# Kernel tuning notes

Measured on AMD Instinct MI355X. Metric: run time of the kernel, lower is better.

Reference implementation:

```python
import jax, jax.numpy as jnp
import numpy as np

B, S_EN, S_FR, EMB, UNITS, V_EN, V_FR = 64, 64, 64, 512, 1024, 32000, 16000


def setup_inputs() -> dict:
    key = jax.random.key(0)
    ks = jax.random.split(key, 16)
    sc = 0.05
    inp = {
        "en": jax.random.randint(ks[0], (B, S_EN), 0, V_EN, dtype=jnp.int32),
        "fr": jax.random.randint(ks[1], (B, S_FR), 0, V_FR, dtype=jnp.int32),
        "valid_len": jax.random.randint(ks[2], (B,), 1, S_EN, dtype=jnp.int32),
        "en_emb": jax.random.normal(ks[3], (V_EN, EMB), jnp.float32) * sc,
        "de_emb": jax.random.normal(ks[4], (V_FR, EMB), jnp.float32) * sc,
        "en_W": jax.random.normal(ks[5], (EMB, 4 * UNITS), jnp.float32) * sc,
        "en_U": jax.random.normal(ks[6], (UNITS, 4 * UNITS), jnp.float32) * sc,
        "en_b": jnp.zeros((4 * UNITS,), jnp.float32),
        "de_W": jax.random.normal(ks[7], (UNITS + EMB, 4 * UNITS), jnp.float32) * sc,
        "de_U": jax.random.normal(ks[8], (UNITS, 4 * UNITS), jnp.float32) * sc,
        "de_b": jnp.zeros((4 * UNITS,), jnp.float32),
        "Wq": jax.random.normal(ks[9], (UNITS, UNITS), jnp.float32) * sc,
        "Wk": jax.random.normal(ks[10], (UNITS, UNITS), jnp.float32) * sc,
        "wv": jax.random.normal(ks[11], (UNITS, 1), jnp.float32) * sc,
        "Wd": jax.random.normal(ks[12], (UNITS, V_FR), jnp.float32) * sc,
        "bd": jnp.zeros((V_FR,), jnp.float32),
    }
    return inp


def _lstm_step(h, c, x, W, Uw, b):
    # keras gate order: i, f, g(candidate), o
    z = x @ W + h @ Uw + b
    i, f, g, o = jnp.split(z, 4, axis=-1)
    c = jax.nn.sigmoid(f) * c + jax.nn.sigmoid(i) * jnp.tanh(g)
    h = jax.nn.sigmoid(o) * jnp.tanh(c)
    return h, c


def reference(en, fr, valid_len, en_emb, de_emb, en_W, en_U, en_b,
              de_W, de_U, de_b, Wq, Wk, wv, Wd, bd):
    b = en.shape[0]
    u = en_U.shape[0]
    # ----- Encode -----
    x_en = en_emb[en]                       # (B, S_en, E)
    h0 = jnp.zeros((b, u), x_en.dtype)

    def enc_step(carry, xt):
        h, c = carry
        h, c = _lstm_step(h, c, xt, en_W, en_U, en_b)
        return (h, c), h

    (h, c), en_o = jax.lax.scan(enc_step, (h0, h0), jnp.swapaxes(x_en, 0, 1))
    en_o = jnp.swapaxes(en_o, 0, 1)         # (B, S_en, U)

    # ----- Decode with additive attention per step -----
    kproj = en_o @ Wk                       # (B, S_en, U), key proj is step-invariant
    pos = jnp.arange(en.shape[1])
    attn_mask = pos[None, :] < valid_len[:, None]   # (B, S_en)
    x_fr = de_emb[fr]                       # (B, S_fr, E)

    def dec_step(carry, xt):
        h, c = carry
        q = h @ Wq                          # (B, U)
        feat = jnp.tanh(q[:, None, :] + kproj)      # (B, S_en, U)
        score = jnp.squeeze(feat @ wv, -1)          # (B, S_en)
        score = jnp.where(attn_mask, score, -1000000.0)
        attn = jax.nn.softmax(score, axis=-1)
        context = jnp.einsum('bs,bsu->bu', attn, en_o)
        x = jnp.concatenate([context, xt], axis=-1)  # (B, U+E)
        h, c = _lstm_step(h, c, x, de_W, de_U, de_b)
        return (h, c), h

    (_, _), hs = jax.lax.scan(dec_step, (h, c), jnp.swapaxes(x_fr, 0, 1))
    logits = jnp.swapaxes(hs, 0, 1) @ Wd + bd       # (B, S_fr, V_fr)
    return logits
```

## Files before the change

### kernel.cpp

```cpp
#include <hip/hip_runtime.h>
#include <math.h>

#define BD    64
#define SEQ   64
#define EMBD  512
#define UNITS 1024
#define NG    4096
#define VFR   16000

typedef __attribute__((ext_vector_type(8))) short bf16x8;
typedef __attribute__((ext_vector_type(4))) float f32x4;

__device__ __forceinline__ float sigm(float x) { return 1.0f / (1.0f + __expf(-x)); }
__device__ __forceinline__ float tanh_f(float x) {
    float e = __expf(2.0f * x);
    return 1.0f - 2.0f / (e + 1.0f);
}
__device__ __forceinline__ unsigned bf16bits(float v) {
    unsigned u = __float_as_uint(v);
    return (u + 0x7FFFu + ((u >> 16) & 1u)) >> 16;
}
__device__ __forceinline__ float bf2f(short s) {
    return __uint_as_float(((unsigned)(unsigned short)s) << 16);
}
__device__ __forceinline__ void split2(float v, short& h, short& l) {
    unsigned hb = bf16bits(v);
    float hv = __uint_as_float(hb << 16);
    h = (short)hb;
    l = (short)bf16bits(v - hv);
}

__device__ __forceinline__ void gbar(int* cnt, int* gen, int nb) {
    __threadfence();
    __syncthreads();
    if (threadIdx.x == 0) {
        int g = __hip_atomic_load(gen, __ATOMIC_RELAXED, __HIP_MEMORY_SCOPE_AGENT);
        if (atomicAdd(cnt, 1) == nb - 1) {
            __hip_atomic_store(cnt, 0, __ATOMIC_RELAXED, __HIP_MEMORY_SCOPE_AGENT);
            __hip_atomic_store(gen, g + 1, __ATOMIC_RELEASE, __HIP_MEMORY_SCOPE_AGENT);
        } else {
            while (__hip_atomic_load(gen, __ATOMIC_RELAXED, __HIP_MEMORY_SCOPE_AGENT) == g)
                __builtin_amdgcn_s_sleep(8);
        }
    }
    __syncthreads();
    __threadfence();
}

__global__ __launch_bounds__(64) void zero16(int* p) {
    if (threadIdx.x < 16) p[threadIdx.x] = 0;
}

__global__ __launch_bounds__(256) void gather_bf16(
    const float* __restrict__ emb, const int* __restrict__ idx,
    short* __restrict__ dst, int K)
{
    int row = blockIdx.x;
    int g = idx[row];
    const float* src = emb + (size_t)g * K;
    for (int k = threadIdx.x * 2; k < K; k += 512) {
        float2 v = *(const float2*)&src[k];
        dst[(size_t)row * K + k]     = (short)bf16bits(v.x);
        dst[(size_t)row * K + k + 1] = (short)bf16bits(v.y);
    }
}

template <bool SPLIT>
__global__ __launch_bounds__(256) void transp_split(
    const float* __restrict__ src, int N, int K,
    short* __restrict__ dh, short* __restrict__ dl)
{
    __shared__ float sm[32][33];
    const int tid = threadIdx.x;
    const int nt = blockIdx.x * 32, kt = blockIdx.y * 32;
    {
        int r = tid >> 3, c4 = (tid & 7) * 4;
        float4 v = *(const float4*)&src[(size_t)(kt + r) * N + nt + c4];
        sm[r][c4] = v.x; sm[r][c4 + 1] = v.y; sm[r][c4 + 2] = v.z; sm[r][c4 + 3] = v.w;
    }
    __syncthreads();
    {
        int n = tid >> 3, k4 = (tid & 7) * 4;
        short4 hh, ll;
        short a, b;
        split2(sm[k4 + 0][n], a, b); hh.x = a; ll.x = b;
        split2(sm[k4 + 1][n], a, b); hh.y = a; ll.y = b;
        split2(sm[k4 + 2][n], a, b); hh.z = a; ll.z = b;
        split2(sm[k4 + 3][n], a, b); hh.w = a; ll.w = b;
        *(short4*)&dh[(size_t)(nt + n) * K + kt + k4] = hh;
        if (SPLIT) *(short4*)&dl[(size_t)(nt + n) * K + kt + k4] = ll;
    }
}

__global__ __launch_bounds__(256) void transp_f32(
    const float* __restrict__ src, int N, int K, float* __restrict__ dst)
{
    __shared__ float sm[32][33];
    const int tid = threadIdx.x;
    const int nt = blockIdx.x * 32, kt = blockIdx.y * 32;
    {
        int r = tid >> 3, c4 = (tid & 7) * 4;
        float4 v = *(const float4*)&src[(size_t)(kt + r) * N + nt + c4];
        sm[r][c4] = v.x; sm[r][c4 + 1] = v.y; sm[r][c4 + 2] = v.z; sm[r][c4 + 3] = v.w;
    }
    __syncthreads();
    {
        int n = tid >> 3, k4 = (tid & 7) * 4;
        float4 o;
        o.x = sm[k4 + 0][n]; o.y = sm[k4 + 1][n];
        o.z = sm[k4 + 2][n]; o.w = sm[k4 + 3][n];
        *(float4*)&dst[(size_t)(nt + n) * K + kt + k4] = o;
    }
}

template <int OMODE, bool SA, bool SB>
__global__ __launch_bounds__(256, 2) void gemm_split(
    const short* __restrict__ Ah, const short* __restrict__ Al,
    const short* __restrict__ Bh, const short* __restrict__ Bl,
    const float* __restrict__ bias, void* __restrict__ Cout, int N, int K)
{
    __shared__ short lds[32 * 512];
    const int tid = threadIdx.x;
    const int lane = tid & 63, w = tid >> 6;
    const int bm = blockIdx.y, bn = blockIdx.x;
    const int wm = w & 1, wn = w >> 1;
    const int r15 = lane & 15, q = lane >> 4;

    f32x4 zero4 = {0.f, 0.f, 0.f, 0.f};
    f32x4 acc[4][4];
#pragma unroll
    for (int i = 0; i < 4; ++i)
#pragma unroll
        for (int j = 0; j < 4; ++j) acc[i][j] = zero4;

    const short* gsrc[8];
    bool use[8];
#pragma unroll
    for (int i = 0; i < 8; ++i) {
        int st = w * 8 + i;
        int mat = st >> 4, hl = (st >> 3) & 1, mt = st & 7;
        const short* base = (mat == 0) ? (hl ? Al : Ah) : (hl ? Bl : Bh);
        use[i] = (mat == 0) ? (SA || hl == 0) : (SB || hl == 0);
        int row = ((mat == 0) ? bm : bn) * 128 + mt * 16 + r15;
        gsrc[i] = base + (size_t)row * K + q * 8;
    }

    for (int k0 = 0; k0 < K; k0 += 32) {
        int4 stg[8];
#pragma unroll
        for (int i = 0; i < 8; ++i)
            if (use[i]) stg[i] = *(const int4*)(gsrc[i] + k0);
        __syncthreads();
#pragma unroll
        for (int i = 0; i < 8; ++i)
            if (use[i]) *(int4*)&lds[(size_t)((w * 8 + i) * 64 + lane) * 8] = stg[i];
        __syncthreads();

        bf16x8 ah[4], al[4], bh[4], bl[4];
#pragma unroll
        for (int i = 0; i < 4; ++i) {
            ah[i] = *(const bf16x8*)&lds[(((wm * 4 + i) * 64) + lane) * 8];
            if (SA) al[i] = *(const bf16x8*)&lds[(((8 + wm * 4 + i) * 64) + lane) * 8];
            bh[i] = *(const bf16x8*)&lds[(((16 + wn * 4 + i) * 64) + lane) * 8];
            if (SB) bl[i] = *(const bf16x8*)&lds[(((24 + wn * 4 + i) * 64) + lane) * 8];
        }
#pragma unroll
        for (int i = 0; i < 4; ++i)
#pragma unroll
            for (int j = 0; j < 4; ++j) {
                acc[i][j] = __builtin_amdgcn_mfma_f32_16x16x32_bf16(ah[i], bh[j], acc[i][j], 0, 0, 0);
                if (SA) acc[i][j] = __builtin_amdgcn_mfma_f32_16x16x32_bf16(al[i], bh[j], acc[i][j], 0, 0, 0);
                if (SB) acc[i][j] = __builtin_amdgcn_mfma_f32_16x16x32_bf16(ah[i], bl[j], acc[i][j], 0, 0, 0);
            }
    }

#pragma unroll
    for (int i = 0; i < 4; ++i) {
        int rowbase = bm * 128 + wm * 64 + i * 16 + q * 4;
#pragma unroll
        for (int j = 0; j < 4; ++j) {
            int col = bn * 128 + wn * 64 + j * 16 + r15;
            float bv = bias ? bias[col] : 0.f;
#pragma unroll
            for (int rI = 0; rI < 4; ++rI) {
                int row = rowbase + rI;
                float v = acc[i][j][rI] + bv;
                if (OMODE == 1) {
                    int orow = ((row & 63) << 6) | (row >> 6);
                    ((float*)Cout)[(size_t)orow * N + col] = v;
                } else if (OMODE == 0) {
                    ((float*)Cout)[(size_t)row * N + col] = v;
                } else if (OMODE == 3) {
                    ((float*)Cout)[((size_t)(row & 63) * N + col) * 64 + (row >> 6)] = v;
                } else {
                    ((short*)Cout)[(size_t)row * N + col] = (short)bf16bits(v);
                }
            }
        }
    }
}

__device__ __forceinline__ void accum_hUT(
    float& a0, float& a1, const float* __restrict__ h_ws,
    const float* __restrict__ UT, int n, int b0, int tid,
    float (*hsm)[66])
{
    const float4* ut = (const float4*)&UT[(size_t)n * 1024];
    for (int k0 = 0; k0 < 1024; k0 += 64) {
        float4 uvr[16];
#pragma unroll
        for (int i = 0; i < 16; ++i) uvr[i] = ut[(k0 >> 2) + i];
        __syncthreads();
#pragma unroll
        for (int i = 0; i < 2; ++i) {
            int idx4 = tid * 2 + i;
            int bb = idx4 >> 4, kq = (idx4 & 15) * 4;
            float4 v = *(const float4*)&h_ws[bb * 1024 + k0 + kq];
            hsm[kq + 0][bb] = v.x;
            hsm[kq + 1][bb] = v.y;
            hsm[kq + 2][bb] = v.z;
            hsm[kq + 3][bb] = v.w;
        }
        __syncthreads();
#pragma unroll
        for (int kk4 = 0; kk4 < 16; ++kk4) {
            float4 uv = uvr[kk4];
            float2 h0v = *(const float2*)&hsm[kk4 * 4 + 0][b0];
            float2 h1v = *(const float2*)&hsm[kk4 * 4 + 1][b0];
            float2 h2v = *(const float2*)&hsm[kk4 * 4 + 2][b0];
            float2 h3v = *(const float2*)&hsm[kk4 * 4 + 3][b0];
            a0 += h0v.x * uv.x + h1v.x * uv.y + h2v.x * uv.z + h3v.x * uv.w;
            a1 += h0v.y * uv.x + h1v.y * uv.y + h2v.y * uv.z + h3v.y * uv.w;
        }
    }
}

__device__ __forceinline__ void lstm_gate_phase(
    int t, int blk, int tid, const float* __restrict__ z_ws,
    float* __restrict__ h_ws, float* __restrict__ c_ws,
    short* __restrict__ oh, short* __restrict__ ol)
{
    int g2 = blk * 512 + tid;
    if (g2 < 65536) {
        int b = g2 >> 10, u = g2 & 1023;
        const float* zr = z_ws + b * NG;
        float zi = zr[u], zf = zr[u + 1024], zg = zr[u + 2048], zo = zr[u + 3072];
        float cp = c_ws[g2];
        float cn = sigm(zf) * cp + sigm(zi) * tanh_f(zg);
        float hn = sigm(zo) * tanh_f(cn);
        c_ws[g2] = cn;
        h_ws[g2] = hn;
        short hh, hl;
        split2(hn, hh, hl);
        size_t o = (size_t)(t * 64 + b) * 1024 + u;
        oh[o] = hh;
        ol[o] = hl;
    }
}

__global__ __launch_bounds__(512, 2) void encoder_persist(
    const short* __restrict__ xW,
    const float* __restrict__ UT,
    float* __restrict__ h_ws, float* __restrict__ c_ws, float* __restrict__ z_ws,
    short* __restrict__ eo_h, short* __restrict__ eo_l,
    int* cnt, int* gen)
{
    __shared__ float hsm[64][66];
    const int tid = threadIdx.x;
    const int blk = blockIdx.x;
    {
        int g = blk * 512 + tid;
        if (g < 65536) h_ws[g] = 0.f;
        else c_ws[g - 65536] = 0.f;
    }
    gbar(cnt, gen, 256);
    const int c16 = tid & 15, bg = tid >> 4;
    const int n = blk * 16 + c16;
    const int b0 = bg * 2;
    for (int t = 0; t < SEQ; ++t) {
        float a0 = bf2f(xW[(size_t)(b0 * 64 + t) * NG + n]);
        float a1 = bf2f(xW[(size_t)((b0 + 1) * 64 + t) * NG + n]);
        accum_hUT(a0, a1, h_ws, UT, n, b0, tid, hsm);
        z_ws[b0 * NG + n] = a0;
        z_ws[(b0 + 1) * NG + n] = a1;
        gbar(cnt, gen, 256);
        lstm_gate_phase(t, blk, tid, z_ws, h_ws, c_ws, eo_h, eo_l);
        gbar(cnt, gen, 256);
    }
}

__global__ __launch_bounds__(512, 2) void decoder_persist(
    const short* __restrict__ xW,
    const float* __restrict__ UT,
    const float* __restrict__ Wq, const float* __restrict__ wv,
    const float* __restrict__ kproj,
    const float* __restrict__ EOT,
    const int* __restrict__ valid_len,
    float* __restrict__ h_ws, float* __restrict__ c_ws, float* __restrict__ z_ws,
    float* __restrict__ q_ws, float* __restrict__ sc_ws,
    short* __restrict__ hs_h, short* __restrict__ hs_l,
    int* cnt, int* gen)
{
    __shared__ float hsm[64][66];
    __shared__ float attn_sm[64][68];
    __shared__ float redq[64][8][4];
    const int tid = threadIdx.x;
    const int blk = blockIdx.x;

    for (int t = 0; t < SEQ; ++t) {
        {
            const int b = tid & 63;
            const int p8 = tid >> 6;
            const int kbase = p8 * 128;
            const int u0 = blk * 4;
            float ax = 0.f, ay = 0.f, az = 0.f, aw = 0.f;
            const float* hrow = h_ws + b * 1024 + kbase;
            const float* wbase = Wq + (size_t)kbase * 1024 + u0;
#pragma unroll 8
            for (int k = 0; k < 128; k += 4) {
                float4 hv = *(const float4*)&hrow[k];
                float4 w0 = *(const float4*)&wbase[(size_t)(k + 0) * 1024];
                float4 w1 = *(const float4*)&wbase[(size_t)(k + 1) * 1024];
                float4 w2 = *(const float4*)&wbase[(size_t)(k + 2) * 1024];
                float4 w3 = *(const float4*)&wbase[(size_t)(k + 3) * 1024];
                ax += hv.x * w0.x + hv.y * w1.x + hv.z * w2.x + hv.w * w3.x;
                ay += hv.x * w0.y + hv.y * w1.y + hv.z * w2.y + hv.w * w3.y;
                az += hv.x * w0.z + hv.y * w1.z + hv.z * w2.z + hv.w * w3.z;
                aw += hv.x * w0.w + hv.y * w1.w + hv.z * w2.w + hv.w * w3.w;
            }
            redq[b][p8][0] = ax; redq[b][p8][1] = ay;
            redq[b][p8][2] = az; redq[b][p8][3] = aw;
            __syncthreads();
            if (tid < 64) {
                float sx = 0.f, sy = 0.f, sz = 0.f, sw = 0.f;
#pragma unroll
                for (int p = 0; p < 8; ++p) {
                    sx += redq[tid][p][0]; sy += redq[tid][p][1];
                    sz += redq[tid][p][2]; sw += redq[tid][p][3];
                }
                float4 o = {sx, sy, sz, sw};
                *(float4*)&q_ws[tid * 1024 + u0] = o;
            }
        }
        gbar(cnt, gen, 256);
        {
            const int p = tid >> 5, l32 = tid & 31;
            const int pair = blk * 16 + p;
            const int b = pair & 63, s = pair >> 6;
            const float* kp = kproj + (size_t)pair * 1024;
            const float* qp = q_ws + b * 1024;
            float a = 0.f;
#pragma unroll
            for (int j = 0; j < 8; ++j) {
                int k = j * 128 + l32 * 4;
                float4 kv = *(const float4*)&kp[k];
                float4 qv = *(const float4*)&qp[k];
                float4 w4 = *(const float4*)&wv[k];
                a += w4.x * tanh_f(qv.x + kv.x);
                a += w4.y * tanh_f(qv.y + kv.y);
                a += w4.z * tanh_f(qv.z + kv.z);
                a += w4.w * tanh_f(qv.w + kv.w);
            }
#pragma unroll
            for (int off = 16; off; off >>= 1) a += __shfl_xor(a, off, 64);
            if (l32 == 0) sc_ws[b * 64 + s] = a;
        }
        gbar(cnt, gen, 256);
        {
            if (tid < 64) {
                const int b = tid;
                const int vl = valid_len[b];
                float mx = -1e30f;
                for (int s = 0; s < 64; ++s) {
                    float v = (s < vl) ? sc_ws[b * 64 + s] : -1000000.0f;
                    attn_sm[b][s] = v;
                    mx = fmaxf(mx, v);
                }
                float sum = 0.f;
                for (int s = 0; s < 64; ++s) {
                    float e = __expf(attn_sm[b][s] - mx);
                    attn_sm[b][s] = e;
                    sum += e;
                }
                float r = 1.f / sum;
                for (int s = 0; s < 64; ++s) attn_sm[b][s] *= r;
            }
            __syncthreads();
            const int c16 = tid & 15, bg = tid >> 4;
            const int n = blk * 16 + c16;
            const int b0 = bg * 2;
            float a0 = bf2f(xW[(size_t)(b0 * 64 + t) * NG + n]);
            float a1 = bf2f(xW[(size_t)((b0 + 1) * 64 + t) * NG + n]);
            const float4* e0 = (const float4*)&EOT[((size_t)b0 * 4096 + n) * 64];
            const float4* e1 = e0 + 65536;
            const float4* w0p = (const float4*)&attn_sm[b0][0];
            const float4* w1p = (const float4*)&attn_sm[b0 + 1][0];
#pragma unroll
            for (int s4 = 0; s4 < 16; ++s4) {
                float4 v0 = e0[s4], v1 = e1[s4];
                float4 x0 = w0p[s4], x1 = w1p[s4];
                a0 += v0.x * x0.x + v0.y * x0.y + v0.z * x0.z + v0.w * x0.w;
                a1 += v1.x * x1.x + v1.y * x1.y + v1.z * x1.z + v1.w * x1.w;
            }
            accum_hUT(a0, a1, h_ws, UT, n, b0, tid, hsm);
            z_ws[b0 * NG + n] = a0;
            z_ws[(b0 + 1) * NG + n] = a1;
        }
        gbar(cnt, gen, 256);
        lstm_gate_phase(t, blk, tid, z_ws, h_ws, c_ws, hs_h, hs_l);
        gbar(cnt, gen, 256);
    }
}

extern "C" void kernel_launch(void* const* d_in, const int* in_sizes, int n_in,
                              void* d_out, int out_size, void* d_ws, size_t ws_size,
                              hipStream_t stream)
{
    const int*   en        = (const int*)d_in[0];
    const int*   fr        = (const int*)d_in[1];
    const int*   valid_len = (const int*)d_in[2];
    const float* en_emb    = (const float*)d_in[3];
    const float* de_emb    = (const float*)d_in[4];
    const float* en_W      = (const float*)d_in[5];
    const float* en_U      = (const float*)d_in[6];
    const float* en_b      = (const float*)d_in[7];
    const float* de_W      = (const float*)d_in[8];
    const float* de_U      = (const float*)d_in[9];
    const float* de_b      = (const float*)d_in[10];
    const float* Wq        = (const float*)d_in[11];
    const float* Wk        = (const float*)d_in[12];
    const float* wv        = (const float*)d_in[13];
    const float* Wd        = (const float*)d_in[14];
    const float* bd        = (const float*)d_in[15];
    float* out = (float*)d_out;
    char*  ws  = (char*)d_ws;

    float* ENUT  = (float*)(ws + 0);
    float* EOT   = (float*)(ws + 0);
    short* WDT_H = (short*)(ws + 0);
    short* WDT_L = (short*)(ws + 33554432);
    short* XWEN  = (short*)(ws + 67108864);
    float* KPROJ = (float*)(ws + 67108864);
    float* DEUT  = (float*)(ws + 83886080);
    short* XWFR  = (short*)(ws + 100663296);
    short* XEN   = (short*)(ws + 134217728);
    short* XFR   = (short*)(ws + 138412032);
    short* WCT_H = (short*)(ws + 134217728);
    short* WCT_L = (short*)(ws + 142606336);
    short* HS_H  = (short*)(ws + 134217728);
    short* HS_L  = (short*)(ws + 142606336);
    short* ENWT  = (short*)(ws + 150994944);
    short* WXT   = (short*)(ws + 155189248);
    short* EO_H  = (short*)(ws + 150994944);
    short* EO_L  = (short*)(ws + 159383552);
    short* WKT_H = (short*)(ws + 167772160);
    short* WKT_L = (short*)(ws + 169869312);
    float* ZWS   = (float*)(ws + 171966464);
    float* HWS   = (float*)(ws + 173015040);
    float* CWS   = (float*)(ws + 173277184);
    float* QWS   = (float*)(ws + 173539328);
    float* SCWS  = (float*)(ws + 173801472);
    int*   BAR   = (int*)(ws + 173817856);

    zero16<<<1, 64, 0, stream>>>(BAR);

    gather_bf16<<<4096, 256, 0, stream>>>(en_emb, en, XEN, EMBD);
    gather_bf16<<<4096, 256, 0, stream>>>(de_emb, fr, XFR, EMBD);
    transp_split<false><<<dim3(128, 16), 256, 0, stream>>>(en_W, NG, EMBD, ENWT, nullptr);
    transp_split<false><<<dim3(128, 16), 256, 0, stream>>>(de_W + (size_t)UNITS * NG, NG, EMBD, WXT, nullptr);
    transp_f32<<<dim3(128, 32), 256, 0, stream>>>(en_U, NG, UNITS, ENUT);

    gemm_split<2, false, false><<<dim3(32, 32), 256, 0, stream>>>(
        XEN, XEN, ENWT, ENWT, en_b, XWEN, NG, EMBD);
    gemm_split<2, false, false><<<dim3(32, 32), 256, 0, stream>>>(
        XFR, XFR, WXT, WXT, de_b, XWFR, NG, EMBD);

    transp_split<true><<<dim3(128, 32), 256, 0, stream>>>(de_W, NG, UNITS, WCT_H, WCT_L);

    encoder_persist<<<256, 512, 0, stream>>>(XWEN, ENUT, HWS, CWS, ZWS, EO_H, EO_L, BAR, BAR + 8);

    transp_f32<<<dim3(128, 32), 256, 0, stream>>>(de_U, NG, UNITS, DEUT);

    gemm_split<3, true, true><<<dim3(32, 32), 256, 0, stream>>>(
        EO_H, EO_L, WCT_H, WCT_L, nullptr, EOT, NG, UNITS);

    transp_split<true><<<dim3(32, 32), 256, 0, stream>>>(Wk, UNITS, UNITS, WKT_H, WKT_L);
    gemm_split<0, true, true><<<dim3(8, 32), 256, 0, stream>>>(
        EO_H, EO_L, WKT_H, WKT_L, nullptr, KPROJ, UNITS, UNITS);

    decoder_persist<<<256, 512, 0, stream>>>(
        XWFR, DEUT, Wq, wv, KPROJ, EOT, valid_len,
        HWS, CWS, ZWS, QWS, SCWS, HS_H, HS_L, BAR, BAR + 8);

    transp_split<true><<<dim3(500, 32), 256, 0, stream>>>(Wd, VFR, UNITS, WDT_H, WDT_L);
    gemm_split<1, true, true><<<dim3(125, 32), 256, 0, stream>>>(
        HS_H, HS_L, WDT_H, WDT_L, bd, out, VFR, UNITS);
}
```

Baseline: 46.82 ms.

## Keep recurrent U slices resident in LDS and fuse gates per block

The persistent encoder and decoder kernels now each own four hidden units across all four gates. Each block stages its transposed U columns into shared memory once, instead of re-reading them from global memory every step. The h·U product is computed as a register-tiled 4x4 outer product over LDS-staged h chunks, and the gate nonlinearity is applied inside the same block. This removes the z workspace round trip and one grid barrier per step, and cell state stays in registers. The change also ping-pongs h buffers and moves to 1024-thread blocks with roughly 150-160 KB of LDS. The risks are occupancy limits, since all 256 blocks must be co-resident for the grid barrier, and extra LDS bank pressure.

Measured after the change: 45.00 ms. 1.04x faster.

```diff
diff --git a/kernel.cpp b/kernel.cpp
--- a/kernel.cpp
+++ b/kernel.cpp
@@ -200,159 +200,217 @@
     }
 }
 
-__device__ __forceinline__ void accum_hUT(
-    float& a0, float& a1, const float* __restrict__ h_ws,
-    const float* __restrict__ UT, int n, int b0, int tid,
-    float (*hsm)[66])
-{
-    const float4* ut = (const float4*)&UT[(size_t)n * 1024];
-    for (int k0 = 0; k0 < 1024; k0 += 64) {
-        float4 uvr[16];
-#pragma unroll
-        for (int i = 0; i < 16; ++i) uvr[i] = ut[(k0 >> 2) + i];
-        __syncthreads();
-#pragma unroll
-        for (int i = 0; i < 2; ++i) {
-            int idx4 = tid * 2 + i;
-            int bb = idx4 >> 4, kq = (idx4 & 15) * 4;
-            float4 v = *(const float4*)&h_ws[bb * 1024 + k0 + kq];
-            hsm[kq + 0][bb] = v.x;
-            hsm[kq + 1][bb] = v.y;
-            hsm[kq + 2][bb] = v.z;
-            hsm[kq + 3][bb] = v.w;
-        }
-        __syncthreads();
-#pragma unroll
-        for (int kk4 = 0; kk4 < 16; ++kk4) {
-            float4 uv = uvr[kk4];
-            float2 h0v = *(const float2*)&hsm[kk4 * 4 + 0][b0];
-            float2 h1v = *(const float2*)&hsm[kk4 * 4 + 1][b0];
-            float2 h2v = *(const float2*)&hsm[kk4 * 4 + 2][b0];
-            float2 h3v = *(const float2*)&hsm[kk4 * 4 + 3][b0];
-            a0 += h0v.x * uv.x + h1v.x * uv.y + h2v.x * uv.z + h3v.x * uv.w;
-            a1 += h0v.y * uv.x + h1v.y * uv.y + h2v.y * uv.z + h3v.y * uv.w;
-        }
-    }
-}
-
-__device__ __forceinline__ void lstm_gate_phase(
-    int t, int blk, int tid, const float* __restrict__ z_ws,
-    float* __restrict__ h_ws, float* __restrict__ c_ws,
+
+#define UCHT_OFF 0
+#define UNI_OFF  65536
+#define ATTN_OFF (65536 + 69632)
+#define ZSM_OFF  (65536 + 69632 + 17408)
+#define ENC_SM   (65536 + 69632 + 4160)
+#define DEC_SM   (65536 + 69632 + 17408 + 4160)
+
+__device__ __forceinline__ void stage_ut(const float* __restrict__ UT,
+                                         float* __restrict__ uchT,
+                                         int n, int nl, int tid)
+{
+    const float* src = UT + (size_t)n * 1024;
+    for (int j = 0; j < 16; ++j) {
+        int k = (tid & 63) + j * 64;
+        uchT[k * 16 + nl] = src[k];
+    }
+}
+
+__device__ __forceinline__ void stage_h(const float* __restrict__ hr,
+                                        float* __restrict__ hch, int c, int tid)
+{
+    const int b = tid >> 4, k0 = (tid & 15) * 16;
+    const float4* s = (const float4*)&hr[b * 1024 + c * 256 + k0];
+    float4 v0 = s[0], v1 = s[1], v2 = s[2], v3 = s[3];
+    float* d = &hch[b * 260 + k0];
+    *(float4*)&d[0]  = v0; *(float4*)&d[4]  = v1;
+    *(float4*)&d[8]  = v2; *(float4*)&d[12] = v3;
+}
+
+__device__ __forceinline__ void hU_chunk(const float* __restrict__ uchT,
+                                         const float* __restrict__ hch,
+                                         int c, int nq, int bq, int w, float* acc)
+{
+#pragma unroll
+    for (int kk4 = 0; kk4 < 4; ++kk4) {
+        const int kl = w * 16 + kk4 * 4;
+        const int kg = c * 256 + kl;
+        float4 hv0 = *(const float4*)&hch[(0 * 16 + bq) * 260 + kl];
+        float4 hv1 = *(const float4*)&hch[(1 * 16 + bq) * 260 + kl];
+        float4 hv2 = *(const float4*)&hch[(2 * 16 + bq) * 260 + kl];
+        float4 hv3 = *(const float4*)&hch[(3 * 16 + bq) * 260 + kl];
+#pragma unroll
+        for (int dk = 0; dk < 4; ++dk) {
+            float4 uv = *(const float4*)&uchT[(kg + dk) * 16 + nq * 4];
+            float h0 = ((const float*)&hv0)[dk];
+            float h1 = ((const float*)&hv1)[dk];
+            float h2 = ((const float*)&hv2)[dk];
+            float h3 = ((const float*)&hv3)[dk];
+            acc[0]  += uv.x * h0; acc[1]  += uv.x * h1; acc[2]  += uv.x * h2; acc[3]  += uv.x * h3;
+            acc[4]  += uv.y * h0; acc[5]  += uv.y * h1; acc[6]  += uv.y * h2; acc[7]  += uv.y * h3;
+            acc[8]  += uv.z * h0; acc[9]  += uv.z * h1; acc[10] += uv.z * h2; acc[11] += uv.z * h3;
+            acc[12] += uv.w * h0; acc[13] += uv.w * h1; acc[14] += uv.w * h2; acc[15] += uv.w * h3;
+        }
+    }
+}
+
+__device__ __forceinline__ void gates_phase(int t, int blk, int tid,
+    const float* __restrict__ zsm, float& creg, float* __restrict__ hw,
     short* __restrict__ oh, short* __restrict__ ol)
 {
-    int g2 = blk * 512 + tid;
-    if (g2 < 65536) {
-        int b = g2 >> 10, u = g2 & 1023;
-        const float* zr = z_ws + b * NG;
-        float zi = zr[u], zf = zr[u + 1024], zg = zr[u + 2048], zo = zr[u + 3072];
-        float cp = c_ws[g2];
-        float cn = sigm(zf) * cp + sigm(zi) * tanh_f(zg);
-        float hn = sigm(zo) * tanh_f(cn);
-        c_ws[g2] = cn;
-        h_ws[g2] = hn;
-        short hh, hl;
-        split2(hn, hh, hl);
-        size_t o = (size_t)(t * 64 + b) * 1024 + u;
-        oh[o] = hh;
-        ol[o] = hl;
-    }
-}
-
-__global__ __launch_bounds__(512, 2) void encoder_persist(
+    const int ul = tid >> 6, b = tid & 63, u = blk * 4 + ul;
+    float zi = zsm[(0 + ul) * 65 + b];
+    float zf = zsm[(4 + ul) * 65 + b];
+    float zg = zsm[(8 + ul) * 65 + b];
+    float zo = zsm[(12 + ul) * 65 + b];
+    float cn = sigm(zf) * creg + sigm(zi) * tanh_f(zg);
+    float hn = sigm(zo) * tanh_f(cn);
+    creg = cn;
+    hw[b * 1024 + u] = hn;
+    short hh, hl;
+    split2(hn, hh, hl);
+    size_t o = (size_t)(t * 64 + b) * 1024 + u;
+    oh[o] = hh;
+    ol[o] = hl;
+}
+
+__global__ __launch_bounds__(1024, 4) void encoder_persist(
     const short* __restrict__ xW,
     const float* __restrict__ UT,
-    float* __restrict__ h_ws, float* __restrict__ c_ws, float* __restrict__ z_ws,
+    float* __restrict__ h0, float* __restrict__ h1, float* __restrict__ c_ws,
     short* __restrict__ eo_h, short* __restrict__ eo_l,
     int* cnt, int* gen)
 {
-    __shared__ float hsm[64][66];
-    const int tid = threadIdx.x;
-    const int blk = blockIdx.x;
-    {
-        int g = blk * 512 + tid;
-        if (g < 65536) h_ws[g] = 0.f;
-        else c_ws[g - 65536] = 0.f;
-    }
+    __shared__ __align__(16) char SM[ENC_SM];
+    float* uchT = (float*)(SM + UCHT_OFF);
+    float* UNI  = (float*)(SM + UNI_OFF);
+    float* zsm  = (float*)(SM + UNI_OFF + 69632);
+    const int tid = threadIdx.x, blk = blockIdx.x;
+    const int nl = tid >> 6, b63 = tid & 63;
+    const int n = blk * 4 + (nl & 3) + 1024 * (nl >> 2);
+    const int nq = tid & 3, bq = (tid >> 2) & 15, w = tid >> 6;
+
+    stage_ut(UT, uchT, n, nl, tid);
+    { int g = blk * 1024 + tid; if (g < 65536) h0[g] = 0.f; }
+    float creg = 0.f;
+    __syncthreads();
     gbar(cnt, gen, 256);
-    const int c16 = tid & 15, bg = tid >> 4;
-    const int n = blk * 16 + c16;
-    const int b0 = bg * 2;
+
     for (int t = 0; t < SEQ; ++t) {
-        float a0 = bf2f(xW[(size_t)(b0 * 64 + t) * NG + n]);
-        float a1 = bf2f(xW[(size_t)((b0 + 1) * 64 + t) * NG + n]);
-        accum_hUT(a0, a1, h_ws, UT, n, b0, tid, hsm);
-        z_ws[b0 * NG + n] = a0;
-        z_ws[(b0 + 1) * NG + n] = a1;
+        const float* hr = (t & 1) ? h1 : h0;
+        float* hw = (t & 1) ? h0 : h1;
+        float* hch = UNI;
+        float* red = UNI;
+        float xwv = bf2f(xW[(size_t)(b63 * 64 + t) * NG + n]);
+        float acc[16];
+#pragma unroll
+        for (int i = 0; i < 16; ++i) acc[i] = 0.f;
+
+        stage_h(hr, hch, 0, tid);
+        __syncthreads();
+        for (int c = 0; c < 4; ++c) {
+            hU_chunk(uchT, hch, c, nq, bq, w, acc);
+            __syncthreads();
+            if (c < 3) { stage_h(hr, hch, c + 1, tid); __syncthreads(); }
+        }
+#pragma unroll
+        for (int jn = 0; jn < 4; ++jn)
+#pragma unroll
+            for (int jb = 0; jb < 4; ++jb)
+                red[((nq * 4 + jn) * 64 + jb * 16 + bq) * 17 + w] = acc[jn * 4 + jb];
+        __syncthreads();
+        float s = 0.f;
+#pragma unroll
+        for (int j = 0; j < 16; ++j) s += red[tid * 17 + j];
+        zsm[nl * 65 + b63] = s + xwv;
+        __syncthreads();
+        if (tid < 256) {
+            gates_phase(t, blk, tid, zsm, creg, hw, eo_h, eo_l);
+            if (t == SEQ - 1) c_ws[(tid & 63) * 1024 + blk * 4 + (tid >> 6)] = creg;
+        }
         gbar(cnt, gen, 256);
-        lstm_gate_phase(t, blk, tid, z_ws, h_ws, c_ws, eo_h, eo_l);
-        gbar(cnt, gen, 256);
-    }
-}
-
-__global__ __launch_bounds__(512, 2) void decoder_persist(
+    }
+}
+
+__global__ __launch_bounds__(1024, 4) void decoder_persist(
     const short* __restrict__ xW,
     const float* __restrict__ UT,
     const float* __restrict__ Wq, const float* __restrict__ wv,
     const float* __restrict__ kproj,
     const float* __restrict__ EOT,
     const int* __restrict__ valid_len,
-    float* __restrict__ h_ws, float* __restrict__ c_ws, float* __restrict__ z_ws,
+    float* __restrict__ h0, float* __restrict__ h1, const float* __restrict__ c_ws,
     float* __restrict__ q_ws, float* __restrict__ sc_ws,
     short* __restrict__ hs_h, short* __restrict__ hs_l,
     int* cnt, int* gen)
 {
-    __shared__ float hsm[64][66];
-    __shared__ float attn_sm[64][68];
-    __shared__ float redq[64][8][4];
-    const int tid = threadIdx.x;
-    const int blk = blockIdx.x;
+    __shared__ __align__(16) char SM[DEC_SM];
+    float* uchT = (float*)(SM + UCHT_OFF);
+    float* UNI  = (float*)(SM + UNI_OFF);
+    float* attn = (float*)(SM + ATTN_OFF);
+    float* zsm  = (float*)(SM + ZSM_OFF);
+    const int tid = threadIdx.x, blk = blockIdx.x;
+    const int nl = tid >> 6, b63 = tid & 63;
+    const int n = blk * 4 + (nl & 3) + 1024 * (nl >> 2);
+    const int nq = tid & 3, bq = (tid >> 2) & 15, w = tid >> 6;
+
+    stage_ut(UT, uchT, n, nl, tid);
+    float creg = (tid < 256) ? c_ws[(tid & 63) * 1024 + blk * 4 + (tid >> 6)] : 0.f;
+    __syncthreads();
 
     for (int t = 0; t < SEQ; ++t) {
+        const float* hr = (t & 1) ? h1 : h0;
+        float* hw = (t & 1) ? h0 : h1;
+
         {
-            const int b = tid & 63;
-            const int p8 = tid >> 6;
-            const int kbase = p8 * 128;
+            float* redq = UNI;
+            const int p = tid >> 6;
+            const int kbase = p * 64;
             const int u0 = blk * 4;
             float ax = 0.f, ay = 0.f, az = 0.f, aw = 0.f;
-            const float* hrow = h_ws + b * 1024 + kbase;
-            const float* wbase = Wq + (size_t)kbase * 1024 + u0;
-#pragma unroll 8
-            for (int k = 0; k < 128; k += 4) {
+            const float* hrow = hr + b63 * 1024 + kbase;
+            const float* wb = Wq + (size_t)kbase * 1024 + u0;
+#pragma unroll 4
+            for (int k = 0; k < 64; k += 4) {
                 float4 hv = *(const float4*)&hrow[k];
-                float4 w0 = *(const float4*)&wbase[(size_t)(k + 0) * 1024];
-                float4 w1 = *(const float4*)&wbase[(size_t)(k + 1) * 1024];
-                float4 w2 = *(const float4*)&wbase[(size_t)(k + 2) * 1024];
-                float4 w3 = *(const float4*)&wbase[(size_t)(k + 3) * 1024];
+                float4 w0 = *(const float4*)&wb[(size_t)(k + 0) * 1024];
+                float4 w1 = *(const float4*)&wb[(size_t)(k + 1) * 1024];
+                float4 w2 = *(const float4*)&wb[(size_t)(k + 2) * 1024];
+                float4 w3 = *(const float4*)&wb[(size_t)(k + 3) * 1024];
                 ax += hv.x * w0.x + hv.y * w1.x + hv.z * w2.x + hv.w * w3.x;
                 ay += hv.x * w0.y + hv.y * w1.y + hv.z * w2.y + hv.w * w3.y;
                 az += hv.x * w0.z + hv.y * w1.z + hv.z * w2.z + hv.w * w3.z;
                 aw += hv.x * w0.w + hv.y * w1.w + hv.z * w2.w + hv.w * w3.w;
             }
-            redq[b][p8][0] = ax; redq[b][p8][1] = ay;
-            redq[b][p8][2] = az; redq[b][p8][3] = aw;
+            float4 o = {ax, ay, az, aw};
+            *(float4*)&redq[(b63 * 17 + p) * 4] = o;
             __syncthreads();
             if (tid < 64) {
                 float sx = 0.f, sy = 0.f, sz = 0.f, sw = 0.f;
 #pragma unroll
-                for (int p = 0; p < 8; ++p) {
-                    sx += redq[tid][p][0]; sy += redq[tid][p][1];
-                    sz += redq[tid][p][2]; sw += redq[tid][p][3];
+                for (int p2 = 0; p2 < 16; ++p2) {
+                    float4 v = *(const float4*)&redq[(tid * 17 + p2) * 4];
+                    sx += v.x; sy += v.y; sz += v.z; sw += v.w;
                 }
-                float4 o = {sx, sy, sz, sw};
-                *(float4*)&q_ws[tid * 1024 + u0] = o;
+                float4 qo = {sx, sy, sz, sw};
+                *(float4*)&q_ws[tid * 1024 + u0] = qo;
             }
         }
         gbar(cnt, gen, 256);
+
         {
-            const int p = tid >> 5, l32 = tid & 31;
+            const int p = tid >> 6, l = tid & 63;
             const int pair = blk * 16 + p;
-            const int b = pair & 63, s = pair >> 6;
+            const int bb = pair & 63, ss = pair >> 6;
             const float* kp = kproj + (size_t)pair * 1024;
-            const float* qp = q_ws + b * 1024;
+            const float* qp = q_ws + bb * 1024;
             float a = 0.f;
 #pragma unroll
-            for (int j = 0; j < 8; ++j) {
-                int k = j * 128 + l32 * 4;
+            for (int j = 0; j < 4; ++j) {
+                int k = j * 256 + l * 4;
                 float4 kv = *(const float4*)&kp[k];
                 float4 qv = *(const float4*)&qp[k];
                 float4 w4 = *(const float4*)&wv[k];
@@ -362,52 +420,67 @@
                 a += w4.w * tanh_f(qv.w + kv.w);
             }
 #pragma unroll
-            for (int off = 16; off; off >>= 1) a += __shfl_xor(a, off, 64);
-            if (l32 == 0) sc_ws[b * 64 + s] = a;
+            for (int off = 32; off; off >>= 1) a += __shfl_xor(a, off, 64);
+            if (l == 0) sc_ws[bb * 64 + ss] = a;
         }
         gbar(cnt, gen, 256);
+
         {
+            float* hch = UNI;
+            float* red = UNI;
+            float xwv = bf2f(xW[(size_t)(b63 * 64 + t) * NG + n]);
+            float acc[16];
+#pragma unroll
+            for (int i = 0; i < 16; ++i) acc[i] = 0.f;
+
+            stage_h(hr, hch, 0, tid);
             if (tid < 64) {
-                const int b = tid;
-                const int vl = valid_len[b];
+                const int bb = tid;
+                const int vl = valid_len[bb];
                 float mx = -1e30f;
-                for (int s = 0; s < 64; ++s) {
-                    float v = (s < vl) ? sc_ws[b * 64 + s] : -1000000.0f;
-                    attn_sm[b][s] = v;
+                for (int s2 = 0; s2 < 64; ++s2) {
+                    float v = (s2 < vl) ? sc_ws[bb * 64 + s2] : -1000000.0f;
+                    attn[bb * 68 + s2] = v;
                     mx = fmaxf(mx, v);
                 }
                 float sum = 0.f;
-                for (int s = 0; s < 64; ++s) {
-                    float e = __expf(attn_sm[b][s] - mx);
-                    attn_sm[b][s] = e;
+                for (int s2 = 0; s2 < 64; ++s2) {
+                    float e = __expf(attn[bb * 68 + s2] - mx);
+                    attn[bb * 68 + s2] = e;
                     sum += e;
                 }
                 float r = 1.f / sum;
-                for (int s = 0; s < 64; ++s) attn_sm[b][s] *= r;
+                for (int s2 = 0; s2 < 64; ++s2) attn[bb * 68 + s2] *= r;
             }
             __syncthreads();
-            const int c16 = tid & 15, bg = tid >> 4;
-            const int n = blk * 16 + c16;
-            const int b0 = bg * 2;
-            float a0 = bf2f(xW[(size_t)(b0 * 64 + t) * NG + n]);
-            float a1 = bf2f(xW[(size_t)((b0 + 1) * 64 + t) * NG + n]);
-            const float4* e0 = (const float4*)&EOT[((size_t)b0 * 4096 + n) * 64];
-            const float4* e1 = e0 + 65536;
-            const float4* w0p = (const float4*)&attn_sm[b0][0];
-            const float4* w1p = (const float4*)&attn_sm[b0 + 1][0];
-#pragma unroll
-            for (int s4 = 0; s4 < 16; ++s4) {
-                float4 v0 = e0[s4], v1 = e1[s4];
-                float4 x0 = w0p[s4], x1 = w1p[s4];
-                a0 += v0.x * x0.x + v0.y * x0.y + v0.z * x0.z + v0.w * x0.w;
-                a1 += v1.x * x1.x + v1.y * x1.y + v1.z * x1.z + v1.w * x1.w;
-            }
-            accum_hUT(a0, a1, h_ws, UT, n, b0, tid, hsm);
-            z_ws[b0 * NG + n] = a0;
-            z_ws[(b0 + 1) * NG + n] = a1;
-        }
-        gbar(cnt, gen, 256);
-        lstm_gate_phase(t, blk, tid, z_ws, h_ws, c_ws, hs_h, hs_l);
+
+            float cx0 = 0.f, cx1 = 0.f, cx2 = 0.f, cx3 = 0.f;
+            const float* ebase = EOT + ((size_t)b63 * 4096 + n) * 64;
+            for (int c = 0; c < 4; ++c) {
+#pragma unroll
+                for (int j = 0; j < 4; ++j) {
+                    float4 ev = *(const float4*)&ebase[c * 16 + j * 4];
+                    float4 av = *(const float4*)&attn[b63 * 68 + c * 16 + j * 4];
+                    cx0 += ev.x * av.x; cx1 += ev.y * av.y;
+                    cx2 += ev.z * av.z; cx3 += ev.w * av.w;
+                }
+                hU_chunk(uchT, hch, c, nq, bq, w, acc);
+                __syncthreads();
+                if (c < 3) { stage_h(hr, hch, c + 1, tid); __syncthreads(); }
+            }
+#pragma unroll
+            for (int jn = 0; jn < 4; ++jn)
+#pragma unroll
+                for (int jb = 0; jb < 4; ++jb)
+                    red[((nq * 4 + jn) * 64 + jb * 16 + bq) * 17 + w] = acc[jn * 4 + jb];
+            __syncthreads();
+            float s = 0.f;
+#pragma unroll
+            for (int j = 0; j < 16; ++j) s += red[tid * 17 + j];
+            zsm[nl * 65 + b63] = s + xwv + ((cx0 + cx1) + (cx2 + cx3));
+            __syncthreads();
+            if (tid < 256) gates_phase(t, blk, tid, zsm, creg, hw, hs_h, hs_l);
+        }
         gbar(cnt, gen, 256);
     }
 }
@@ -445,6 +518,7 @@
     short* XWFR  = (short*)(ws + 100663296);
     short* XEN   = (short*)(ws + 134217728);
     short* XFR   = (short*)(ws + 138412032);
+    float* HENC1 = (float*)(ws + 134217728);
     short* WCT_H = (short*)(ws + 134217728);
     short* WCT_L = (short*)(ws + 142606336);
     short* HS_H  = (short*)(ws + 134217728);
@@ -453,9 +527,9 @@
     short* WXT   = (short*)(ws + 155189248);
     short* EO_H  = (short*)(ws + 150994944);
     short* EO_L  = (short*)(ws + 159383552);
+    float* HDEC1 = (float*)(ws + 150994944);
     short* WKT_H = (short*)(ws + 167772160);
     short* WKT_L = (short*)(ws + 169869312);
-    float* ZWS   = (float*)(ws + 171966464);
     float* HWS   = (float*)(ws + 173015040);
     float* CWS   = (float*)(ws + 173277184);
     float* QWS   = (float*)(ws + 173539328);
@@ -475,10 +549,10 @@
     gemm_split<2, false, false><<<dim3(32, 32), 256, 0, stream>>>(
         XFR, XFR, WXT, WXT, de_b, XWFR, NG, EMBD);
 
+    encoder_persist<<<256, 1024, 0, stream>>>(
+        XWEN, ENUT, HWS, HENC1, CWS, EO_H, EO_L, BAR, BAR + 8);
+
     transp_split<true><<<dim3(128, 32), 256, 0, stream>>>(de_W, NG, UNITS, WCT_H, WCT_L);
-
-    encoder_persist<<<256, 512, 0, stream>>>(XWEN, ENUT, HWS, CWS, ZWS, EO_H, EO_L, BAR, BAR + 8);
-
     transp_f32<<<dim3(128, 32), 256, 0, stream>>>(de_U, NG, UNITS, DEUT);
 
     gemm_split<3, true, true><<<dim3(32, 32), 256, 0, stream>>>(
@@ -488,9 +562,9 @@
     gemm_split<0, true, true><<<dim3(8, 32), 256, 0, stream>>>(
         EO_H, EO_L, WKT_H, WKT_L, nullptr, KPROJ, UNITS, UNITS);
 
-    decoder_persist<<<256, 512, 0, stream>>>(
+    decoder_persist<<<256, 1024, 0, stream>>>(
         XWFR, DEUT, Wq, wv, KPROJ, EOT, valid_len,
-        HWS, CWS, ZWS, QWS, SCWS, HS_H, HS_L, BAR, BAR + 8);
+        HWS, HDEC1, CWS, QWS, SCWS, HS_H, HS_L, BAR, BAR + 8);
 
     transp_split<true><<<dim3(500, 32), 256, 0, stream>>>(Wd, VFR, UNITS, WDT_H, WDT_L);
     gemm_split<1, true, true><<<dim3(125, 32), 256, 0, stream>>>(
```
